# Optimization experiments

Measured on AMD Instinct MI355X. Metric: run time of the kernel, lower is better.

Reference implementation:

```python
import jax, jax.numpy as jnp
import numpy as np

L, N, K = 512, 64, 38      # seq_len, batch, input feature size
E, H = 1024, 1024          # embed_size, hidden_size
NUM_LAYERS = 3
C = 38                     # num_classes


def setup_inputs() -> dict:
    key = jax.random.key(0)
    ks = jax.random.split(key, 9)
    s_e = 1.0 / np.sqrt(K)
    s_h = 1.0 / np.sqrt(H)
    return {
        "inputs": jax.random.normal(ks[0], (L, N, K), jnp.float32),
        "emb_W": jax.random.uniform(ks[1], (E, K), jnp.float32, -s_e, s_e),
        "emb_b": jnp.zeros((E,), jnp.float32),
        # GRU weights, PyTorch layout: gates ordered (r, z, n) along 3H axis
        "w_ih": jax.random.uniform(ks[2], (NUM_LAYERS, 3 * H, E), jnp.float32, -s_h, s_h),
        "w_hh": jax.random.uniform(ks[3], (NUM_LAYERS, 3 * H, H), jnp.float32, -s_h, s_h),
        "b_ih": jax.random.uniform(ks[4], (NUM_LAYERS, 3 * H), jnp.float32, -s_h, s_h),
        "b_hh": jax.random.uniform(ks[5], (NUM_LAYERS, 3 * H), jnp.float32, -s_h, s_h),
        "out_W": jax.random.uniform(ks[6], (C, H), jnp.float32, -s_h, s_h),
        "out_b": jnp.zeros((C,), jnp.float32),
    }


def _gru_layer(x, w_ih, w_hh, b_ih, b_hh):
    # x: (L, N, in_dim) -> outputs (L, N, H), final hidden (N, H)
    # Precompute all input projections as one big GEMM: (L, N, 3H)
    xg = jnp.einsum('lni,gi->lng', x, w_ih) + b_ih
    h0 = jnp.zeros((x.shape[1], H), x.dtype)

    def step(h, xg_t):
        hg = h @ w_hh.T + b_hh                      # (N, 3H)
        xr, xz, xn = jnp.split(xg_t, 3, axis=-1)
        hr, hz, hn = jnp.split(hg, 3, axis=-1)
        r = jax.nn.sigmoid(xr + hr)
        z = jax.nn.sigmoid(xz + hz)
        n = jnp.tanh(xn + r * hn)
        h_new = (1.0 - z) * n + z * h
        return h_new, h_new

    h_last, outs = jax.lax.scan(step, h0, xg)
    return outs, h_last


def reference(inputs, emb_W, emb_b, w_ih, w_hh, b_ih, b_hh, out_W, out_b):
    # embedding: Linear(K -> E), applied per timestep
    x = jnp.einsum('lnk,ek->lne', inputs, emb_W) + emb_b  # (L, N, E)
    for l in range(NUM_LAYERS):  # fixed structural loop over layers
        x, _ = _gru_layer(x, w_ih[l], w_hh[l], b_ih[l], b_hh[l])
    # output projection: Linear(H -> C)
    logit = jnp.einsum('lnh,ch->lnc', x, out_W) + out_b    # (L, N, C)
    return logit
```

## Files before the change

### kernel.cpp

```cpp
#include <hip/hip_runtime.h>
#include <hip/hip_fp16.h>
#include <stdint.h>
#include <stddef.h>

typedef _Float16 f16;
typedef _Float16 f16x8 __attribute__((ext_vector_type(8)));
typedef float f32x4 __attribute__((ext_vector_type(4)));

#define SEQL 512
#define NBATCH 64
#define KIN 38
#define KPAD 64
#define EMB 1024
#define HID 1024
#define G3 3072
#define MALL (SEQL*NBATCH)
#define NCLS 38
#define WPAD 1032


__global__ void k_cvt(const float* __restrict__ s, f16* __restrict__ d, long n) {
  long i = (long)blockIdx.x * blockDim.x + threadIdx.x;
  long stride = (long)gridDim.x * blockDim.x;
  for (; i < n; i += stride) d[i] = (f16)s[i];
}

__global__ void k_zero(int* __restrict__ p, int n) {
  int i = blockIdx.x * 256 + threadIdx.x;
  if (i < n) p[i] = 0;
}

__global__ void k_outw_pad(const float* __restrict__ s, f16* __restrict__ d) {
  int i = blockIdx.x * 256 + threadIdx.x;
  if (i >= 128 * 1024) return;
  int r = i >> 10, c = i & 1023;
  d[i] = (r < NCLS) ? (f16)s[r * 1024 + c] : (f16)0.f;
}

__global__ void k_cvt_in(const float* __restrict__ s, f16* __restrict__ d) {
  int i = blockIdx.x * 256 + threadIdx.x;
  if (i >= MALL * KPAD) return;
  int m = i >> 6, k = i & 63;
  d[i] = (k < KIN) ? (f16)s[m * KIN + k] : (f16)0.f;
}

__global__ void k_prep_w0(const float* __restrict__ wih0, const float* __restrict__ embW,
                          f16* __restrict__ w0) {
  int i = blockIdx.x * 256 + threadIdx.x;
  if (i >= G3 * KPAD) return;
  int g = i >> 6, k = i & 63;
  float sacc = 0.f;
  if (k < KIN) {
    for (int e = 0; e < EMB; ++e) sacc += wih0[g * EMB + e] * embW[e * KIN + k];
  }
  w0[i] = (f16)sacc;
}

__global__ void k_prep_b0(const float* __restrict__ wih0, const float* __restrict__ embB,
                          const float* __restrict__ bih0, float* __restrict__ b0) {
  int g = blockIdx.x * 256 + threadIdx.x;
  if (g >= G3) return;
  float sacc = bih0[g];
  for (int e = 0; e < EMB; ++e) sacc += wih0[g * EMB + e] * embB[e];
  b0[g] = sacc;
}


__global__ __launch_bounds__(256) void k_gemm(
    const f16* __restrict__ A, const f16* __restrict__ B,
    const float* __restrict__ bias,
    f16* __restrict__ C16, float* __restrict__ C32,
    int K, int nvalid, int ldc) {
  __shared__ f16 As[128][40];
  __shared__ f16 Bs[128][40];
  const int tid = threadIdx.x;
  const long brow = (long)blockIdx.x * 128;
  const long bcol = (long)blockIdx.y * 128;
  const int w = tid >> 6, lane = tid & 63;
  const int lr = lane & 15, kg = lane >> 4;
  const int wr = w >> 1, wc = w & 1;

  f32x4 acc[4][4] = {};

  for (int kk = 0; kk < K; kk += 32) {
    __syncthreads();
#pragma unroll
    for (int p = 0; p < 2; ++p) {
      int idx = p * 256 + tid;
      int row = idx >> 2, seg = idx & 3;
      *(float4*)(&As[row][seg * 8]) = *(const float4*)(&A[(brow + row) * K + kk + seg * 8]);
      *(float4*)(&Bs[row][seg * 8]) = *(const float4*)(&B[(bcol + row) * K + kk + seg * 8]);
    }
    __syncthreads();
    f16x8 af[4], bf[4];
#pragma unroll
    for (int i = 0; i < 4; ++i) af[i] = *(const f16x8*)(&As[wr * 64 + i * 16 + lr][kg * 8]);
#pragma unroll
    for (int j = 0; j < 4; ++j) bf[j] = *(const f16x8*)(&Bs[wc * 64 + j * 16 + lr][kg * 8]);
#pragma unroll
    for (int i = 0; i < 4; ++i)
#pragma unroll
      for (int j = 0; j < 4; ++j)
        acc[i][j] = __builtin_amdgcn_mfma_f32_16x16x32_f16(af[i], bf[j], acc[i][j], 0, 0, 0);
  }

#pragma unroll
  for (int j = 0; j < 4; ++j) {
    int col = (int)bcol + wc * 64 + j * 16 + lr;
    float bv = (col < nvalid) ? bias[col] : 0.f;
#pragma unroll
    for (int i = 0; i < 4; ++i) {
#pragma unroll
      for (int r = 0; r < 4; ++r) {
        long row = brow + wr * 64 + i * 16 + kg * 4 + r;
        float v = acc[i][j][r] + bv;
        if (C16) C16[row * ldc + col] = (f16)v;
        else if (col < nvalid) C32[row * ldc + col] = v;
      }
    }
  }
}


__global__ __launch_bounds__(256) void k_rnn(
    f16* __restrict__ xseq,
    f16* __restrict__ hbuf,
    const f16* __restrict__ xg,
    const f16* __restrict__ whhl,
    const float* __restrict__ bhhl,
    int t0, int T, int* __restrict__ cnt) {
  __shared__ f16 wlds[48 * WPAD];
  const int g = blockIdx.x, j0 = g * 16, tid = threadIdx.x;
  const int w = tid >> 6, lane = tid & 63, lr = lane & 15, kg = lane >> 4;

  for (int idx = tid; idx < 48 * 128; idx += 256) {
    int row = idx >> 7, seg = idx & 127;
    int gt = row >> 4, r = row & 15;
    *(f16x8*)&wlds[row * WPAD + seg * 8] =
        *(const f16x8*)&whhl[(size_t)((gt << 10) + j0 + r) * HID + seg * 8];
  }
  __syncthreads();

  const int j = j0 + lr;
  const float br = bhhl[j], bz = bhhl[1024 + j], bn = bhhl[2048 + j];
  const f16* wr_ = &wlds[(0 * 16 + lr) * WPAD];
  const f16* wz_ = &wlds[(1 * 16 + lr) * WPAD];
  const f16* wn_ = &wlds[(2 * 16 + lr) * WPAD];

  for (int tt = 0; tt < T; ++tt) {
    const int t = t0 + tt;
    f32x4 ar = {}, az = {}, an = {};
    if (t > 0) {
      const f16* hb = hbuf + (((t & 1) ^ 1) ? (size_t)(64 * HID) : 0);
      const f16* hbase = hb + (16 * w + lr) * 16 + (kg & 1) * 8 + (kg >> 1) * 1024;
      const int ko0 = kg * 8;
#pragma unroll 8
      for (int kc = 0; kc < 32; ++kc) {
        f16x8 a = *(const f16x8*)(hbase + kc * 2048);
        int ko = kc * 32 + ko0;
        ar = __builtin_amdgcn_mfma_f32_16x16x32_f16(a, *(const f16x8*)(wr_ + ko), ar, 0, 0, 0);
        az = __builtin_amdgcn_mfma_f32_16x16x32_f16(a, *(const f16x8*)(wz_ + ko), az, 0, 0, 0);
        an = __builtin_amdgcn_mfma_f32_16x16x32_f16(a, *(const f16x8*)(wn_ + ko), an, 0, 0, 0);
      }
    }
    const f16* hbp = hbuf + (((t & 1) ^ 1) ? (size_t)(64 * HID) : 0) + g * 1024;
    f16* hbn = hbuf + ((t & 1) ? (size_t)(64 * HID) : 0) + g * 1024;
    f16* xrow = xseq + (size_t)t * (NBATCH * HID);
    const f16* xgt = xg + (size_t)tt * NBATCH * G3;
#pragma unroll
    for (int r = 0; r < 4; ++r) {
      int m = 16 * w + kg * 4 + r;
      float xr = (float)xgt[m * G3 + j];
      float xz = (float)xgt[m * G3 + 1024 + j];
      float xn = (float)xgt[m * G3 + 2048 + j];
      float hp = (t > 0) ? (float)hbp[m * 16 + lr] : 0.f;
      float rr = 1.f / (1.f + __expf(-(xr + ar[r] + br)));
      float zz = 1.f / (1.f + __expf(-(xz + az[r] + bz)));
      float pre = xn + rr * (an[r] + bn);
      float nn = 2.f / (1.f + __expf(-2.f * pre)) - 1.f;
      float hv = (1.f - zz) * nn + zz * hp;
      hbn[m * 16 + lr] = (f16)hv;
      xrow[m * HID + j] = (f16)hv;
    }
    __syncthreads();
    if (tid == 0) {
      __hip_atomic_fetch_add(&cnt[t], 1, __ATOMIC_RELEASE, __HIP_MEMORY_SCOPE_AGENT);
      while (__hip_atomic_load(&cnt[t], __ATOMIC_ACQUIRE, __HIP_MEMORY_SCOPE_AGENT) < 64) {
        __builtin_amdgcn_s_sleep(1);
      }
    }
    __syncthreads();
  }
}


extern "C" void kernel_launch(void* const* d_in, const int* in_sizes, int n_in,
                              void* d_out, int out_size, void* d_ws, size_t ws_size,
                              hipStream_t stream) {
  const float* in   = (const float*)d_in[0];
  const float* embW = (const float*)d_in[1];
  const float* embB = (const float*)d_in[2];
  const float* wih  = (const float*)d_in[3];
  const float* whh  = (const float*)d_in[4];
  const float* bih  = (const float*)d_in[5];
  const float* bhh  = (const float*)d_in[6];
  const float* outW = (const float*)d_in[7];
  const float* outB = (const float*)d_in[8];
  float* out = (float*)d_out;

  char* ws = (char*)d_ws;
  size_t off = 0;
  auto alloc = [&](size_t bytes) -> void* {
    void* p = ws + off; off += (bytes + 255) & ~(size_t)255; return p;
  };
  f16* whhL   = (f16*)alloc((size_t)G3 * HID * 2);
  f16* wihL   = (f16*)alloc((size_t)G3 * HID * 2);
  f16* w016   = (f16*)alloc((size_t)G3 * KPAD * 2);
  f16* outw16 = (f16*)alloc(128UL * HID * 2);
  float* b0   = (float*)alloc((size_t)G3 * 4);
  f16* in16   = (f16*)alloc((size_t)MALL * KPAD * 2);
  f16* xseq   = (f16*)alloc((size_t)MALL * HID * 2);
  f16* hbuf   = (f16*)alloc(2UL * NBATCH * HID * 2);
  int* cnt    = (int*)alloc(3UL * SEQL * 4);
  size_t fixed = off;

  int T = 128;
  while (T > 2 && fixed + ((size_t)T * NBATCH * G3 * 2 + 256) > ws_size) T >>= 1;
  f16* xg = (f16*)alloc((size_t)T * NBATCH * G3 * 2);
  if (off > ws_size) return;
  const int NCHUNK = SEQL / T;

  k_zero<<<(3 * SEQL + 255) / 256, 256, 0, stream>>>(cnt, 3 * SEQL);
  k_outw_pad<<<512, 256, 0, stream>>>(outW, outw16);
  k_cvt_in<<<(MALL * KPAD + 255) / 256, 256, 0, stream>>>(in, in16);
  k_prep_w0<<<(G3 * KPAD + 255) / 256, 256, 0, stream>>>(wih, embW, w016);
  k_prep_b0<<<(G3 + 255) / 256, 256, 0, stream>>>(wih, embB, bih, b0);

  for (int l = 0; l < 3; ++l) {
    k_cvt<<<2048, 256, 0, stream>>>(whh + (size_t)l * G3 * HID, whhL, (long)G3 * HID);
    if (l > 0)
      k_cvt<<<2048, 256, 0, stream>>>(wih + (size_t)l * G3 * EMB, wihL, (long)G3 * HID);

    for (int c = 0; c < NCHUNK; ++c) {
      if (l == 0)
        k_gemm<<<dim3(T * NBATCH / 128, G3 / 128), 256, 0, stream>>>(
            in16 + (size_t)c * T * NBATCH * KPAD, w016, b0, xg, nullptr, KPAD, G3, G3);
      else
        k_gemm<<<dim3(T * NBATCH / 128, G3 / 128), 256, 0, stream>>>(
            xseq + (size_t)c * T * NBATCH * HID, wihL, bih + l * G3, xg, nullptr, HID, G3, G3);
      k_rnn<<<64, 256, 0, stream>>>(xseq, hbuf, xg, whhL, bhh + l * G3,
                                    c * T, T, cnt + l * SEQL);
    }
  }
  k_gemm<<<dim3(MALL / 128, 1), 256, 0, stream>>>(xseq, outw16, outB, nullptr, out,
                                                  HID, NCLS, NCLS);
}
```

Before: 16.48 ms.

## Replace atomic-counter grid barrier with per-block flags and prefetch xg inputs

Replaces the per-timestep global counter barrier (atomic add, then spin by one thread, then a second __syncthreads) with per-block monotonic flags on padded cache lines. Each wavefront polls all 64 flags with a wave-wide __all before reading the previous hidden state. This removes one block-level barrier and contention on a single counter, and lets blocks start as soon as their producers publish. It also prefetches the next timestep's input-gate values into registers after signalling, so their load latency is hidden behind the wait. In exchange, every wavefront now polls 64 flags with no sleep.

```diff
diff --git a/kernel.cpp b/kernel.cpp
--- a/kernel.cpp
+++ b/kernel.cpp
@@ -17,6 +17,7 @@
 #define MALL (SEQL*NBATCH)
 #define NCLS 38
 #define WPAD 1032
+#define FS 32
 
 
 __global__ void k_cvt(const float* __restrict__ s, f16* __restrict__ d, long n) {
@@ -128,7 +129,8 @@
     const f16* __restrict__ xg,
     const f16* __restrict__ whhl,
     const float* __restrict__ bhhl,
-    int t0, int T, int* __restrict__ cnt) {
+    int t0, int T, int base,
+    int* __restrict__ flags) {
   __shared__ f16 wlds[48 * WPAD];
   const int g = blockIdx.x, j0 = g * 16, tid = threadIdx.x;
   const int w = tid >> 6, lane = tid & 63, lr = lane & 15, kg = lane >> 4;
@@ -147,49 +149,68 @@
   const f16* wz_ = &wlds[(1 * 16 + lr) * WPAD];
   const f16* wn_ = &wlds[(2 * 16 + lr) * WPAD];
 
+  f16 pxr[4], pxz[4], pxn[4];
+#pragma unroll
+  for (int r = 0; r < 4; ++r) {
+    int m = 16 * w + kg * 4 + r;
+    pxr[r] = xg[m * G3 + j];
+    pxz[r] = xg[m * G3 + 1024 + j];
+    pxn[r] = xg[m * G3 + 2048 + j];
+  }
+
   for (int tt = 0; tt < T; ++tt) {
     const int t = t0 + tt;
     f32x4 ar = {}, az = {}, an = {};
+    float hp4[4] = {0.f, 0.f, 0.f, 0.f};
     if (t > 0) {
-      const f16* hb = hbuf + (((t & 1) ^ 1) ? (size_t)(64 * HID) : 0);
+      const int target = base + t;
+      int v;
+      do {
+        v = __hip_atomic_load(&flags[lane * FS], __ATOMIC_ACQUIRE, __HIP_MEMORY_SCOPE_AGENT);
+      } while (!__all(v >= target));
+      const f16* hb = hbuf + (((t & 1) ^ 1) ? (size_t)(NBATCH * HID) : 0);
+      const f16* hbp = hb + g * 1024;
+#pragma unroll
+      for (int r = 0; r < 4; ++r)
+        hp4[r] = (float)hbp[(16 * w + kg * 4 + r) * 16 + lr];
       const f16* hbase = hb + (16 * w + lr) * 16 + (kg & 1) * 8 + (kg >> 1) * 1024;
-      const int ko0 = kg * 8;
 #pragma unroll 8
       for (int kc = 0; kc < 32; ++kc) {
         f16x8 a = *(const f16x8*)(hbase + kc * 2048);
-        int ko = kc * 32 + ko0;
+        int ko = kc * 32 + kg * 8;
         ar = __builtin_amdgcn_mfma_f32_16x16x32_f16(a, *(const f16x8*)(wr_ + ko), ar, 0, 0, 0);
         az = __builtin_amdgcn_mfma_f32_16x16x32_f16(a, *(const f16x8*)(wz_ + ko), az, 0, 0, 0);
         an = __builtin_amdgcn_mfma_f32_16x16x32_f16(a, *(const f16x8*)(wn_ + ko), an, 0, 0, 0);
       }
     }
-    const f16* hbp = hbuf + (((t & 1) ^ 1) ? (size_t)(64 * HID) : 0) + g * 1024;
-    f16* hbn = hbuf + ((t & 1) ? (size_t)(64 * HID) : 0) + g * 1024;
+    f16* hbn = hbuf + ((t & 1) ? (size_t)(NBATCH * HID) : 0) + g * 1024;
     f16* xrow = xseq + (size_t)t * (NBATCH * HID);
-    const f16* xgt = xg + (size_t)tt * NBATCH * G3;
 #pragma unroll
     for (int r = 0; r < 4; ++r) {
       int m = 16 * w + kg * 4 + r;
-      float xr = (float)xgt[m * G3 + j];
-      float xz = (float)xgt[m * G3 + 1024 + j];
-      float xn = (float)xgt[m * G3 + 2048 + j];
-      float hp = (t > 0) ? (float)hbp[m * 16 + lr] : 0.f;
+      float xr = (float)pxr[r], xz = (float)pxz[r], xn = (float)pxn[r];
       float rr = 1.f / (1.f + __expf(-(xr + ar[r] + br)));
       float zz = 1.f / (1.f + __expf(-(xz + az[r] + bz)));
       float pre = xn + rr * (an[r] + bn);
       float nn = 2.f / (1.f + __expf(-2.f * pre)) - 1.f;
-      float hv = (1.f - zz) * nn + zz * hp;
+      float hv = (1.f - zz) * nn + zz * hp4[r];
       hbn[m * 16 + lr] = (f16)hv;
       xrow[m * HID + j] = (f16)hv;
     }
     __syncthreads();
-    if (tid == 0) {
-      __hip_atomic_fetch_add(&cnt[t], 1, __ATOMIC_RELEASE, __HIP_MEMORY_SCOPE_AGENT);
-      while (__hip_atomic_load(&cnt[t], __ATOMIC_ACQUIRE, __HIP_MEMORY_SCOPE_AGENT) < 64) {
-        __builtin_amdgcn_s_sleep(1);
+    if (tid == 0)
+      __hip_atomic_store(&flags[g * FS], base + t + 1, __ATOMIC_RELEASE,
+                         __HIP_MEMORY_SCOPE_AGENT);
+    if (tt + 1 < T) {
+      const f16* xgt = xg + (size_t)(tt + 1) * NBATCH * G3;
+#pragma unroll
+      for (int r = 0; r < 4; ++r) {
+        int m = 16 * w + kg * 4 + r;
+        pxr[r] = xgt[m * G3 + j];
+        pxz[r] = xgt[m * G3 + 1024 + j];
+        pxn[r] = xgt[m * G3 + 2048 + j];
       }
     }
-    __syncthreads();
   }
 }
 
@@ -221,7 +242,7 @@
   f16* in16   = (f16*)alloc((size_t)MALL * KPAD * 2);
   f16* xseq   = (f16*)alloc((size_t)MALL * HID * 2);
   f16* hbuf   = (f16*)alloc(2UL * NBATCH * HID * 2);
-  int* cnt    = (int*)alloc(3UL * SEQL * 4);
+  int* flags  = (int*)alloc(64UL * FS * 4);
   size_t fixed = off;
 
   int T = 128;
@@ -230,7 +251,7 @@
   if (off > ws_size) return;
   const int NCHUNK = SEQL / T;
 
-  k_zero<<<(3 * SEQL + 255) / 256, 256, 0, stream>>>(cnt, 3 * SEQL);
+  k_zero<<<(64 * FS + 255) / 256, 256, 0, stream>>>(flags, 64 * FS);
   k_outw_pad<<<512, 256, 0, stream>>>(outW, outw16);
   k_cvt_in<<<(MALL * KPAD + 255) / 256, 256, 0, stream>>>(in, in16);
   k_prep_w0<<<(G3 * KPAD + 255) / 256, 256, 0, stream>>>(wih, embW, w016);
@@ -249,7 +270,7 @@
         k_gemm<<<dim3(T * NBATCH / 128, G3 / 128), 256, 0, stream>>>(
             xseq + (size_t)c * T * NBATCH * HID, wihL, bih + l * G3, xg, nullptr, HID, G3, G3);
       k_rnn<<<64, 256, 0, stream>>>(xseq, hbuf, xg, whhL, bhh + l * G3,
-                                    c * T, T, cnt + l * SEQL);
+                                    c * T, T, l * SEQL, flags);
     }
   }
   k_gemm<<<dim3(MALL / 128, 1), 256, 0, stream>>>(xseq, outw16, outB, nullptr, out,
```

Measured after the change: 16.75 ms. About the same (+1.6%).
